# Performance work log

Measured on AMD Instinct MI355X. Metric: run time of the kernel, lower is better.

The kernel has to match this reference:

```python
import jax, jax.numpy as jnp
import numpy as np

B, S, D, H = 2, 2048, 1024, 16
HD = D // H
EPS = 1e-8
LN_EPS = 1e-5


def setup_inputs() -> dict:
    key = jax.random.key(0)
    ks = jax.random.split(key, 12)
    std = 0.02
    inp = {}
    inp["x"] = jax.random.normal(ks[0], (B, S, D), jnp.float32)
    # q/k/v/out projections (stored (in, out); y = x @ W + b)
    inp["Wq"] = jax.random.normal(ks[1], (D, D), jnp.float32) * std
    inp["bq"] = jnp.zeros((D,), jnp.float32)
    inp["Wk"] = jax.random.normal(ks[2], (D, D), jnp.float32) * std
    inp["bk"] = jnp.zeros((D,), jnp.float32)
    inp["Wv"] = jax.random.normal(ks[3], (D, D), jnp.float32) * std
    inp["bv"] = jnp.zeros((D,), jnp.float32)
    inp["Wo"] = jax.random.normal(ks[4], (D, D), jnp.float32) * std
    inp["bo"] = jnp.zeros((D,), jnp.float32)
    # 4 DeltaResidualBlocks stacked on axis 0: [q, k, v, out]
    inp["dWk"] = jax.random.normal(ks[5], (4, D, D), jnp.float32) * 0.01  # k_proj, no bias
    inp["dbw"] = jnp.zeros((4, D), jnp.float32)                           # beta_proj weight (init zeros)
    inp["dbb"] = jnp.full((4,), -4.0, jnp.float32)                        # beta_proj bias
    inp["dWv"] = jax.random.normal(ks[6], (4, D), jnp.float32) * 0.02     # v_proj weight (d_v=1)
    inp["dbv"] = jnp.zeros((4,), jnp.float32)                             # v_proj bias
    inp["ln_g"] = jnp.ones((D,), jnp.float32)
    inp["ln_b"] = jnp.zeros((D,), jnp.float32)
    return inp


def reference(x, Wq, bq, Wk, bk, Wv, bv, Wo, bo, dWk, dbw, dbb, dWv, dbv, ln_g, ln_b):
    def delta(h, v_in, i):
        # DeltaResidualBlock (d_v=1): h + beta * k * (v - k.h)
        k_raw = jnp.einsum('bsd,de->bse', h, dWk[i])
        k = k_raw / (jnp.linalg.norm(k_raw, axis=-1, keepdims=True) + EPS)
        beta = 2.0 * jax.nn.sigmoid(jnp.einsum('bsd,d->bs', h, dbw[i])[..., None] + dbb[i])  # (B,S,1)
        v = jnp.einsum('bsd,d->bs', v_in, dWv[i])[..., None] + dbv[i]                        # (B,S,1)
        k_dot_h = jnp.sum(k * h, axis=-1, keepdims=True)
        return h + beta * k * (v - k_dot_h)

    q = delta(x, x @ Wq + bq, 0)
    k = delta(x, x @ Wk + bk, 1)
    v = delta(x, x @ Wv + bv, 2)

    # (B,S,D) -> (B,H,S,HD)
    q = q.reshape(B, S, H, HD).transpose(0, 2, 1, 3)
    k = k.reshape(B, S, H, HD).transpose(0, 2, 1, 3)
    v = v.reshape(B, S, H, HD).transpose(0, 2, 1, 3)

    scale = HD ** -0.5
    scores = jnp.einsum('bhqd,bhkd->bhqk', q, k) * scale
    attn = jax.nn.softmax(scores, axis=-1)
    out = jnp.einsum('bhqk,bhkd->bhqd', attn, v)
    out = out.transpose(0, 2, 1, 3).reshape(B, S, D)
    out = out @ Wo + bo

    y = delta(x, out, 3)

    # LayerNorm
    mu = jnp.mean(y, axis=-1, keepdims=True)
    var = jnp.mean((y - mu) ** 2, axis=-1, keepdims=True)
    y = (y - mu) / jnp.sqrt(var + LN_EPS) * ln_g + ln_b
    return y
```

## Files before the change

### kernel.cpp

```cpp
#include <hip/hip_runtime.h>

#define BB 2
#define SS 2048
#define DD 1024
#define HH 16
#define HD 64
#define MM (BB*SS)
#define KC 4
#define KT_PER (SS/64/KC)
#define KSTEPS (DD/64)

typedef unsigned short u16;
typedef __attribute__((ext_vector_type(8))) short bf16x8;
typedef __attribute__((ext_vector_type(4))) float f32x4;

typedef __attribute__((address_space(1))) const unsigned int* gas_t;
typedef __attribute__((address_space(3))) unsigned int* las_t;

#ifndef __has_builtin
#define __has_builtin(x) 0
#endif
#if __has_builtin(__builtin_amdgcn_exp2f)
#define EXP2F(x) __builtin_amdgcn_exp2f(x)
#else
#define EXP2F(x) __expf((x)*0.6931471805599453f)
#endif
#define QSCALE 0.18033688011112042f

__device__ __forceinline__ void gl_lds16(const u16* g, u16* l){
  __builtin_amdgcn_global_load_lds((gas_t)g, (las_t)l, 16, 0, 0);
}

__device__ __forceinline__ u16 f2bf(float f){
  unsigned u = __float_as_uint(f);
  u += 0x7FFF + ((u >> 16) & 1);
  return (u16)(u >> 16);
}
__device__ __forceinline__ float bf2f(u16 h){
  return __uint_as_float(((unsigned)h) << 16);
}
__device__ __forceinline__ float dot4f(float4 a, float4 b){
  return a.x*b.x + a.y*b.y + a.z*b.z + a.w*b.w;
}

template <int CTRL>
__device__ __forceinline__ float dppadd(float x){
  int y = __builtin_amdgcn_update_dpp(0, __float_as_int(x), CTRL, 0xF, 0xF, true);
  return x + __int_as_float(y);
}
__device__ __forceinline__ float4 wsum64_f4(float4 v){
  #define DPP_ST(c) v.x=dppadd<c>(v.x); v.y=dppadd<c>(v.y); v.z=dppadd<c>(v.z); v.w=dppadd<c>(v.w);
  DPP_ST(0x111) DPP_ST(0x112) DPP_ST(0x114) DPP_ST(0x118) DPP_ST(0x142) DPP_ST(0x143)
  #undef DPP_ST
  return v;
}
__device__ __forceinline__ float2 wsum64_f2(float2 v){
  #define DPP_ST(c) v.x=dppadd<c>(v.x); v.y=dppadd<c>(v.y);
  DPP_ST(0x111) DPP_ST(0x112) DPP_ST(0x114) DPP_ST(0x118) DPP_ST(0x142) DPP_ST(0x143)
  #undef DPP_ST
  return v;
}

#define SB0() __builtin_amdgcn_sched_barrier(0)
#define SBAR() do { \
  __builtin_amdgcn_sched_barrier(0); \
  __builtin_amdgcn_s_barrier(); \
  __builtin_amdgcn_sched_barrier(0); \
} while (0)

#define NB_CONV 2048
#define NB_TRAN 1024
#define NB_PREC 4100
#define NB_PREP (NB_CONV+NB_TRAN+NB_PREC)
__global__ void prep_kernel(const float* __restrict__ x, u16* __restrict__ xb,
                            const float* __restrict__ dWk, u16* __restrict__ dWkT,
                            const float* __restrict__ Wq_, const float* __restrict__ bq_,
                            const float* __restrict__ Wk_, const float* __restrict__ bk_,
                            const float* __restrict__ Wv_, const float* __restrict__ bv_,
                            const float* __restrict__ Wo_, const float* __restrict__ bo_,
                            const float* __restrict__ dWv, const float* __restrict__ dbv,
                            float* __restrict__ wv, float* __restrict__ cv) {
  int blk = blockIdx.x, t = threadIdx.x;
  if (blk < NB_CONV) {
    size_t idx = ((size_t)blk*256 + t)*8;
    float4 a = *(const float4*)(x + idx);
    float4 b = *(const float4*)(x + idx + 4);
    union { u16 u[8]; uint4 v; } pk;
    pk.u[0]=f2bf(a.x); pk.u[1]=f2bf(a.y); pk.u[2]=f2bf(a.z); pk.u[3]=f2bf(a.w);
    pk.u[4]=f2bf(b.x); pk.u[5]=f2bf(b.y); pk.u[6]=f2bf(b.z); pk.u[7]=f2bf(b.w);
    *(uint4*)(xb + idx) = pk.v;
    return;
  }
  blk -= NB_CONV;
  if (blk < NB_TRAN) {
    int i = blk >> 8, rest = blk & 255;
    int k0 = (rest >> 4) << 6, n0 = (rest & 15) << 6;
    const float* src = dWk + (size_t)i*DD*DD;
    u16* dst = dWkT + (size_t)i*DD*DD;
    __shared__ u16 tr[64*68];
    const int krb = (t >> 4) << 2;
    const int nqb = (t & 15) << 2;
    float4 v0 = *(const float4*)(src + (size_t)(k0+krb+0)*DD + n0 + nqb);
    float4 v1 = *(const float4*)(src + (size_t)(k0+krb+1)*DD + n0 + nqb);
    float4 v2 = *(const float4*)(src + (size_t)(k0+krb+2)*DD + n0 + nqb);
    float4 v3 = *(const float4*)(src + (size_t)(k0+krb+3)*DD + n0 + nqb);
    *(uint2*)(&tr[(nqb+0)*68 + krb]) = make_uint2(
        (unsigned)f2bf(v0.x) | ((unsigned)f2bf(v1.x)<<16),
        (unsigned)f2bf(v2.x) | ((unsigned)f2bf(v3.x)<<16));
    *(uint2*)(&tr[(nqb+1)*68 + krb]) = make_uint2(
        (unsigned)f2bf(v0.y) | ((unsigned)f2bf(v1.y)<<16),
        (unsigned)f2bf(v2.y) | ((unsigned)f2bf(v3.y)<<16));
    *(uint2*)(&tr[(nqb+2)*68 + krb]) = make_uint2(
        (unsigned)f2bf(v0.z) | ((unsigned)f2bf(v1.z)<<16),
        (unsigned)f2bf(v2.z) | ((unsigned)f2bf(v3.z)<<16));
    *(uint2*)(&tr[(nqb+3)*68 + krb]) = make_uint2(
        (unsigned)f2bf(v0.w) | ((unsigned)f2bf(v1.w)<<16),
        (unsigned)f2bf(v2.w) | ((unsigned)f2bf(v3.w)<<16));
    __syncthreads();
    const int n = t >> 2, c = t & 3;
    uint2 r0 = *(uint2*)(&tr[n*68 + c*16 + 0]);
    uint2 r1 = *(uint2*)(&tr[n*68 + c*16 + 4]);
    uint2 r2 = *(uint2*)(&tr[n*68 + c*16 + 8]);
    uint2 r3 = *(uint2*)(&tr[n*68 + c*16 + 12]);
    u16* dp = dst + (size_t)(n0+n)*DD + k0 + c*16;
    *(uint4*)(dp + 0) = make_uint4(r0.x, r0.y, r1.x, r1.y);
    *(uint4*)(dp + 8) = make_uint4(r2.x, r2.y, r3.x, r3.y);
    return;
  }
  blk -= NB_TRAN;
  {
    int i = blk / 1025, row = blk % 1025;
    const float* W    = (i==0)?Wq_:(i==1)?Wk_:(i==2)?Wv_:Wo_;
    const float* bvec = (i==0)?bq_:(i==1)?bk_:(i==2)?bv_:bo_;
    const float* s = dWv + i*DD;
    __shared__ float red[256];
    float acc = 0.f;
    if (row < DD) {
      const float* r = W + (size_t)row * DD;
      for (int e = t; e < DD; e += 256) acc += r[e]*s[e];
    } else {
      for (int e = t; e < DD; e += 256) acc += bvec[e]*s[e];
    }
    red[t] = acc; __syncthreads();
    for (int off=128; off>0; off>>=1){ if(t<off) red[t]+=red[t+off]; __syncthreads(); }
    if (t==0) {
      if (row < DD) wv[i*DD + row] = red[0];
      else          cv[i] = red[0] + dbv[i];
    }
  }
}

__device__ __forceinline__ void stage_half(const u16* __restrict__ g, u16* l,
                                           int k0, int half, int isA,
                                           int wid, int lane) {
  const int lr = lane>>3, lc = lane&7;
  #pragma unroll
  for (int j=0; j<2; j++) {
    const int u = wid*2 + j;
    int grow;
    if (isA) grow = ((u & 8) ? 128 + ((u & 7)<<3) : (u<<3)) + (half<<6);
    else     grow = ((u>>2)<<6) + ((u&3)<<3) + (half<<5);
    gl_lds16(g + (size_t)(grow + lr)*DD + k0 + ((lc^lr)<<3), l + grow*64);
  }
}

__device__ __forceinline__ void lda4(const u16* base, int row0, int q15, int quad,
                                     int sw, bf16x8 (&f)[4][2]) {
  #pragma unroll
  for (int mf=0; mf<4; mf++)
    #pragma unroll
    for (int kk=0; kk<2; kk++)
      f[mf][kk] = *(const bf16x8*)(base + (row0 + mf*16 + q15)*64 + (((kk*4+quad)^sw)<<3));
}
__device__ __forceinline__ void ldb2(const u16* base, int row0, int q15, int quad,
                                     int sw, bf16x8 (&f)[2][2]) {
  #pragma unroll
  for (int nf=0; nf<2; nf++)
    #pragma unroll
    for (int kk=0; kk<2; kk++)
      f[nf][kk] = *(const bf16x8*)(base + (row0 + nf*16 + q15)*64 + (((kk*4+quad)^sw)<<3));
}
__device__ __forceinline__ void quad_mfma(const bf16x8 (&af)[4][2], const bf16x8 (&bfr)[2][2],
                                          f32x4 (&acc)[8][4], int mo, int no) {
  __builtin_amdgcn_s_setprio(1);
  #pragma unroll
  for (int kk=0; kk<2; kk++)
    #pragma unroll
    for (int mf=0; mf<4; mf++)
      #pragma unroll
      for (int nf=0; nf<2; nf++)
        acc[mo+mf][no+nf] = __builtin_amdgcn_mfma_f32_16x16x32_bf16(
            bfr[nf][kk], af[mf][kk], acc[mo+mf][no+nf], 0,0,0);
  __builtin_amdgcn_s_setprio(0);
}

__global__ __launch_bounds__(512, 2) void gemm_dwk_8ph(const u16* __restrict__ xb,
                          const u16* __restrict__ Bt, u16* __restrict__ kraw) {
  const int bid = blockIdx.x;
  const int xcd = bid & 7, rr = bid >> 3;
  const int i = xcd >> 1;
  const int mt = ((xcd & 1) << 3) | (rr & 7);
  const int ntile = rr >> 3;
  const int m0 = mt << 8, n0 = ntile << 8;
  const u16* Ab = xb + (size_t)m0*DD;
  const u16* Bb = Bt + (size_t)i*DD*DD + (size_t)n0*DD;
  u16* C = kraw + (size_t)i*MM*DD;

  const int t = threadIdx.x, wid = t>>6, lane = t&63;
  const int q15 = lane&15, quad = lane>>4, sw = q15&7;
  const int wm = wid>>2, wn = wid&3;
  const int arow = wm<<7, brow = wn<<6;

  __shared__ u16 As[2][256*64];
  __shared__ u16 Bs[2][256*64];

  f32x4 acc[8][4];
  #pragma unroll
  for (int a=0;a<8;a++)
    #pragma unroll
    for (int b2=0;b2<4;b2++) acc[a][b2] = (f32x4){0.f,0.f,0.f,0.f};

  stage_half(Ab, As[0], 0,  0, 1, wid, lane);
  stage_half(Bb, Bs[0], 0,  0, 0, wid, lane);
  stage_half(Bb, Bs[0], 0,  1, 0, wid, lane);
  stage_half(Ab, As[0], 0,  1, 1, wid, lane);
  stage_half(Ab, As[1], 64, 0, 1, wid, lane);
  stage_half(Bb, Bs[1], 64, 0, 0, wid, lane);
  stage_half(Bb, Bs[1], 64, 1, 0, wid, lane);
  SB0();
  asm volatile("s_waitcnt vmcnt(6)" ::: "memory");
  SBAR();

  for (int u=0; u<KSTEPS; ++u) {
    const int cur = u & 1;
    const u16* Ac = As[cur]; const u16* Bc = Bs[cur];
    const int k1 = (u+1 < KSTEPS ? u+1 : KSTEPS-1) << 6;
    const int k2 = (u+2 < KSTEPS ? u+2 : KSTEPS-1) << 6;
    bf16x8 a0[4][2], a1[4][2], b0[2][2], b1[2][2];

    lda4(Ac, arow,    q15, quad, sw, a0);
    ldb2(Bc, brow,    q15, quad, sw, b0);
    ldb2(Bc, brow+32, q15, quad, sw, b1);
    stage_half(Ab, As[cur^1], k1, 1, 1, wid, lane);
    SB0();
    quad_mfma(a0, b0, acc, 0, 0);
    quad_mfma(a0, b1, acc, 0, 2);
    SB0();
    lda4(Ac, arow+64, q15, quad, sw, a1);
    SB0();
    __builtin_amdgcn_s_barrier();
    SB0();
    stage_half(Ab, As[cur], k2, 0, 1, wid, lane);
    stage_half(Bb, Bs[cur], k2, 0, 0, wid, lane);
    stage_half(Bb, Bs[cur], k2, 1, 0, wid, lane);
    SB0();
    quad_mfma(a1, b1, acc, 4, 2);
    quad_mfma(a1, b0, acc, 4, 0);
    SB0();
    asm volatile("s_waitcnt vmcnt(6)" ::: "memory");
    __builtin_amdgcn_s_barrier();
    SB0();
  }

  #pragma unroll
  for (int mf=0; mf<8; mf++) {
    const int m = m0 + arow + mf*16 + q15;
    u16* Crow = C + (size_t)m*DD + n0 + brow;
    #pragma unroll
    for (int nf=0; nf<4; nf++) {
      unsigned u0 = (unsigned)f2bf(acc[mf][nf][0]) | ((unsigned)f2bf(acc[mf][nf][1]) << 16);
      unsigned u1 = (unsigned)f2bf(acc[mf][nf][2]) | ((unsigned)f2bf(acc[mf][nf][3]) << 16);
      *(uint2*)(Crow + nf*16 + quad*4) = make_uint2(u0, u1);
    }
  }
}

__global__ void delta_qkv_kernel(const float* __restrict__ x, const u16* __restrict__ kraw,
                                 const float* __restrict__ dbw, const float* __restrict__ dbb,
                                 const float* __restrict__ wv, const float* __restrict__ cv,
                                 u16* __restrict__ qk, float* __restrict__ Vw) {
  int m = blockIdx.x, t = threadIdx.x, w = t>>6, lane = t&63;
  const float* xr = x + (size_t)m*DD;
  float4 xv = *(const float4*)(xr + t*4);
  __shared__ float4 part[3][4];
  float4 kvs[3];
  #pragma unroll
  for (int i=0;i<3;i++) {
    ushort4 ku = *(const ushort4*)(kraw + (size_t)i*MM*DD + (size_t)m*DD + t*4);
    float4 kv = make_float4(bf2f(ku.x), bf2f(ku.y), bf2f(ku.z), bf2f(ku.w));
    kvs[i] = kv;
    float4 bwv = *(const float4*)(dbw + i*DD + t*4);
    float4 wvv = *(const float4*)(wv  + i*DD + t*4);
    float4 red = make_float4(dot4f(kv,kv), dot4f(kv,xv), dot4f(xv,bwv), dot4f(xv,wvv));
    red = wsum64_f4(red);
    if (lane==63) part[i][w] = red;
  }
  __syncthreads();
  float cc[3];
  #pragma unroll
  for (int i=0;i<3;i++) {
    float4 r0=part[i][0], r1=part[i][1], r2=part[i][2], r3=part[i][3];
    float s0=r0.x+r1.x+r2.x+r3.x, s1=r0.y+r1.y+r2.y+r3.y;
    float s2=r0.z+r1.z+r2.z+r3.z, s3=r0.w+r1.w+r2.w+r3.w;
    float nrmE = sqrtf(s0) + 1e-8f;
    float kdh  = s1 / nrmE;
    float beta = 2.f / (1.f + __expf(-(s2 + dbb[i])));
    float vs   = s3 + cv[i];
    cc[i] = beta * (vs - kdh) / nrmE;
  }
  {
    float c = cc[0]; float4 kv = kvs[0];
    ushort4 ou;
    ou.x = f2bf((xv.x + c*kv.x)*QSCALE); ou.y = f2bf((xv.y + c*kv.y)*QSCALE);
    ou.z = f2bf((xv.z + c*kv.z)*QSCALE); ou.w = f2bf((xv.w + c*kv.w)*QSCALE);
    *(ushort4*)(qk + (size_t)m*DD + t*4) = ou;
  }
  {
    float c = cc[1]; float4 kv = kvs[1];
    ushort4 ou;
    ou.x = f2bf(xv.x + c*kv.x); ou.y = f2bf(xv.y + c*kv.y);
    ou.z = f2bf(xv.z + c*kv.z); ou.w = f2bf(xv.w + c*kv.w);
    *(ushort4*)(qk + (size_t)MM*DD + (size_t)m*DD + t*4) = ou;
  }
  {
    float c = cc[2]; float4 kv = kvs[2];
    float4 vv = make_float4(xv.x + c*kv.x, xv.y + c*kv.y, xv.z + c*kv.z, xv.w + c*kv.w);
    float4 w3 = *(const float4*)(wv + 3*DD + t*4);
    float s = dot4f(vv, w3);
    #pragma unroll
    for (int off=1; off<16; off<<=1) s += __shfl_xor(s, off);
    if ((lane & 15) == 0) {
      int head = t >> 4;
      int b = m >> 11, srow = m & (SS-1);
      Vw[((size_t)(b*HH + head))*SS + srow] = s;
    }
  }
}

__global__ __launch_bounds__(256, 6) void flash_mfma(const u16* __restrict__ qb,
     const u16* __restrict__ kb, const float* __restrict__ Vw,
     float* __restrict__ l_arr, float* __restrict__ pv_arr) {
  const int qt = blockIdx.x, h = blockIdx.y;
  const int b = blockIdx.z >> 2, kc = blockIdx.z & 3;
  const int t = threadIdx.x, w = t>>6, lane = t&63, q15 = lane&15, quad = lane>>4;
  const int lr = lane>>3, lc = lane&7, gsw = lc ^ lr;
  const int sw = q15 & 7;
  __shared__ u16 Ks[3][64*64];
  __shared__ float Vws[KT_PER*64];
  const size_t hb = (size_t)h*HD;
  const u16* kbase = kb + (size_t)(b*SS + kc*KT_PER*64)*DD + hb;
  const float* vwb = Vw + (size_t)(b*HH + h)*SS + kc*KT_PER*64;

  bf16x8 qf[2];
  {
    const u16* qrow = qb + (size_t)(b*SS + qt*64 + w*16 + q15)*DD + hb;
    qf[0] = *(const bf16x8*)(qrow + quad*8);
    qf[1] = *(const bf16x8*)(qrow + 32 + quad*8);
  }
  if (t < KT_PER*64/4) {
    float4 v = *(const float4*)(vwb + t*4);
    *(float4*)(&Vws[t*4]) = v;
  }
  #pragma unroll
  for (int j=0; j<2; j++) {
    int r = (w*2+j)*8 + lr;
    gl_lds16(kbase + (size_t)r*DD + gsw*8, &Ks[0][((w*2+j)*8)*64]);
    gl_lds16(kbase + (size_t)(64 + r)*DD + gsw*8, &Ks[1][((w*2+j)*8)*64]);
  }
  float l_acc = 0.f, pv_acc = 0.f;
  __syncthreads();

  #pragma unroll
  for (int kt=0; kt<KT_PER; kt++) {
    if (kt+2 < KT_PER) {
      #pragma unroll
      for (int j=0; j<2; j++) {
        int r = (w*2+j)*8 + lr;
        gl_lds16(kbase + (size_t)((kt+2)*64 + r)*DD + gsw*8,
                 &Ks[(kt+2)%3][((w*2+j)*8)*64]);
      }
    }
    f32x4 Sacc[4];
    #pragma unroll
    for (int rt=0; rt<4; rt++) Sacc[rt] = (f32x4){0.f,0.f,0.f,0.f};
    #pragma unroll
    for (int kk=0; kk<2; kk++) {
      #pragma unroll
      for (int rt=0; rt<4; rt++) {
        bf16x8 kf = *(bf16x8*)(&Ks[kt%3][(rt*16+q15)*64 + ((kk*4+quad)^sw)*8]);
        Sacc[rt] = __builtin_amdgcn_mfma_f32_16x16x32_bf16(kf, qf[kk], Sacc[rt], 0,0,0);
      }
    }
    #pragma unroll
    for (int rt=0; rt<4; rt++) {
      float4 va = *(const float4*)(&Vws[kt*64 + rt*16 + quad*4]);
      float p0 = EXP2F(fminf(Sacc[rt][0], 30.f));
      float p1 = EXP2F(fminf(Sacc[rt][1], 30.f));
      float p2 = EXP2F(fminf(Sacc[rt][2], 30.f));
      float p3 = EXP2F(fminf(Sacc[rt][3], 30.f));
      l_acc  += (p0 + p1) + (p2 + p3);
      pv_acc += p0*va.x + p1*va.y + p2*va.z + p3*va.w;
    }
    if (kt < KT_PER-1) {
      __builtin_amdgcn_sched_barrier(0);
      if (kt+2 < KT_PER) asm volatile("s_waitcnt vmcnt(2)" ::: "memory");
      else               asm volatile("s_waitcnt vmcnt(0)" ::: "memory");
      __builtin_amdgcn_s_barrier();
      __builtin_amdgcn_sched_barrier(0);
    }
  }
  l_acc  += __shfl_xor(l_acc, 16);  l_acc  += __shfl_xor(l_acc, 32);
  pv_acc += __shfl_xor(pv_acc, 16); pv_acc += __shfl_xor(pv_acc, 32);
  if (quad == 0) {
    int tok = b*SS + qt*64 + w*16 + q15;
    size_t idx = ((size_t)kc*MM + tok)*HH + h;
    l_arr[idx]  = l_acc;
    pv_arr[idx] = pv_acc;
  }
}

__global__ void final_kernel(const float* __restrict__ x, const u16* __restrict__ kraw3,
                             const float* __restrict__ l_arr, const float* __restrict__ pv_arr,
                             const float* __restrict__ dbw, const float* __restrict__ dbb,
                             const float* __restrict__ cv,
                             const float* __restrict__ ln_g, const float* __restrict__ ln_b,
                             float* __restrict__ out) {
  int m = blockIdx.x, t = threadIdx.x, w = t>>6, lane = t&63;
  const float* xr = x     + (size_t)m*DD;
  const u16*   kr = kraw3 + (size_t)m*DD;
  float4 xv  = *(const float4*)(xr + t*4);
  ushort4 ku = *(const ushort4*)(kr + t*4);
  float4 kv  = make_float4(bf2f(ku.x), bf2f(ku.y), bf2f(ku.z), bf2f(ku.w));
  float4 bwv = *(const float4*)(dbw + 3*DD + t*4);
  __shared__ float4 part[4];
  __shared__ float2 part2[4];
  __shared__ float v3s;
  if (t < 16) {
    float lsum = 0.f, psum = 0.f;
    #pragma unroll
    for (int kc=0; kc<KC; kc++) {
      size_t idx = ((size_t)kc*MM + m)*HH + t;
      lsum += l_arr[idx];
      psum += pv_arr[idx];
    }
    float val = psum / lsum;
    #pragma unroll
    for (int off=1; off<16; off<<=1) val += __shfl_xor(val, off);
    if (t==0) v3s = val;
  }
  float4 red = make_float4(dot4f(kv,kv), dot4f(kv,xv), dot4f(xv,bwv), 0.f);
  red = wsum64_f4(red);
  if (lane==63) part[w] = red;
  __syncthreads();
  float4 r0=part[0], r1=part[1], r2=part[2], r3=part[3];
  float s0=r0.x+r1.x+r2.x+r3.x, s1=r0.y+r1.y+r2.y+r3.y, s2=r0.z+r1.z+r2.z+r3.z;
  float nrmE = sqrtf(s0) + 1e-8f;
  float kdh  = s1 / nrmE;
  float beta = 2.f / (1.f + __expf(-(s2 + dbb[3])));
  float v3   = v3s + cv[3];
  float c = beta * (v3 - kdh) / nrmE;
  float y0 = xv.x + c*kv.x, y1 = xv.y + c*kv.y, y2 = xv.z + c*kv.z, y3 = xv.w + c*kv.w;
  float2 rr = make_float2(y0+y1+y2+y3, y0*y0+y1*y1+y2*y2+y3*y3);
  rr = wsum64_f2(rr);
  if (lane==63) part2[w] = rr;
  __syncthreads();
  float ssum = part2[0].x+part2[1].x+part2[2].x+part2[3].x;
  float ssq  = part2[0].y+part2[1].y+part2[2].y+part2[3].y;
  float mu   = ssum * (1.f/DD);
  float var  = ssq * (1.f/DD) - mu*mu;
  float rstd = rsqrtf(var + 1e-5f);
  float4 g  = *(const float4*)(ln_g + t*4);
  float4 bb = *(const float4*)(ln_b + t*4);
  float4 ov;
  ov.x = (y0-mu)*rstd*g.x + bb.x;
  ov.y = (y1-mu)*rstd*g.y + bb.y;
  ov.z = (y2-mu)*rstd*g.z + bb.z;
  ov.w = (y3-mu)*rstd*g.w + bb.w;
  *(float4*)(out + (size_t)m*DD + t*4) = ov;
}

extern "C" void kernel_launch(void* const* d_in, const int* in_sizes, int n_in,
                              void* d_out, int out_size, void* d_ws, size_t ws_size,
                              hipStream_t stream) {
  const float* x    = (const float*)d_in[0];
  const float* Wq_  = (const float*)d_in[1];
  const float* bq_  = (const float*)d_in[2];
  const float* Wk_  = (const float*)d_in[3];
  const float* bk_  = (const float*)d_in[4];
  const float* Wv_  = (const float*)d_in[5];
  const float* bv_  = (const float*)d_in[6];
  const float* Wo_  = (const float*)d_in[7];
  const float* bo_  = (const float*)d_in[8];
  const float* dWk  = (const float*)d_in[9];
  const float* dbw  = (const float*)d_in[10];
  const float* dbb  = (const float*)d_in[11];
  const float* dWv  = (const float*)d_in[12];
  const float* dbv  = (const float*)d_in[13];
  const float* ln_g = (const float*)d_in[14];
  const float* ln_b = (const float*)d_in[15];
  float* out = (float*)d_out;
  char* WS = (char*)d_ws;

  float* wv     = (float*)WS;
  float* cv     = (float*)(WS + 16384);
  u16*   kraw   = (u16*)  (WS + 16640);
  u16*   qk     = (u16*)  (WS + 16640 + (size_t)4*MM*DD*2);
  u16*   dWkT   = (u16*)  (WS + 16640 + (size_t)6*MM*DD*2);
  u16*   xb     = (u16*)  (WS + 16640 + (size_t)6*MM*DD*2 + (size_t)4*DD*DD*2);
  char*  tail   = WS + 16640 + (size_t)6*MM*DD*2 + (size_t)8*DD*DD*2;
  float* Vw     = (float*)tail;
  float* l_arr  = (float*)(tail + (size_t)BB*HH*SS*4);
  float* pv_arr = (float*)(tail + (size_t)BB*HH*SS*4 + (size_t)KC*MM*HH*4);

  prep_kernel<<<NB_PREP, 256, 0, stream>>>(
      x, xb, dWk, dWkT, Wq_,bq_,Wk_,bk_,Wv_,bv_,Wo_,bo_, dWv, dbv, wv, cv);
  gemm_dwk_8ph<<<256, 512, 0, stream>>>(xb, dWkT, kraw);
  delta_qkv_kernel<<<MM, 256, 0, stream>>>(x, kraw, dbw, dbb, wv, cv, qk, Vw);
  flash_mfma<<<dim3(SS/64, HH, BB*KC), 256, 0, stream>>>(
      qk, qk + (size_t)MM*DD, Vw, l_arr, pv_arr);
  final_kernel<<<MM, 256, 0, stream>>>(x, kraw + 3*(size_t)MM*DD, l_arr, pv_arr,
                                       dbw, dbb, cv, ln_g, ln_b, out);
}
```

Before: 219.6 us.

## Split flash key tile across waves instead of query rows, reduce via LDS

Each wave now owns 16 keys of the 64-key tile and computes scores against all 64 query rows. It loads only two K fragments per step instead of eight, while holding four sets of Q fragments in registers. Per-row partial sums from the four waves are combined through shared memory before the global write. The aim is fewer LDS reads per MFMA, paid for with more registers, which is why the occupancy hint drops from 6 to 4 blocks, plus an extra barrier and reduction at the end.

```diff
diff --git a/kernel.cpp b/kernel.cpp
--- a/kernel.cpp
+++ b/kernel.cpp
@@ -337,7 +337,7 @@
   }
 }
 
-__global__ __launch_bounds__(256, 6) void flash_mfma(const u16* __restrict__ qb,
+__global__ __launch_bounds__(256, 4) void flash_mfma(const u16* __restrict__ qb,
      const u16* __restrict__ kb, const float* __restrict__ Vw,
      float* __restrict__ l_arr, float* __restrict__ pv_arr) {
   const int qt = blockIdx.x, h = blockIdx.y;
@@ -347,15 +347,17 @@
   const int sw = q15 & 7;
   __shared__ u16 Ks[3][64*64];
   __shared__ float Vws[KT_PER*64];
+  __shared__ float2 red2[4*64];
   const size_t hb = (size_t)h*HD;
   const u16* kbase = kb + (size_t)(b*SS + kc*KT_PER*64)*DD + hb;
   const float* vwb = Vw + (size_t)(b*HH + h)*SS + kc*KT_PER*64;
 
-  bf16x8 qf[2];
-  {
-    const u16* qrow = qb + (size_t)(b*SS + qt*64 + w*16 + q15)*DD + hb;
-    qf[0] = *(const bf16x8*)(qrow + quad*8);
-    qf[1] = *(const bf16x8*)(qrow + 32 + quad*8);
+  bf16x8 qf[4][2];
+  #pragma unroll
+  for (int qt2=0; qt2<4; qt2++) {
+    const u16* qrow = qb + (size_t)(b*SS + qt*64 + qt2*16 + q15)*DD + hb;
+    qf[qt2][0] = *(const bf16x8*)(qrow + quad*8);
+    qf[qt2][1] = *(const bf16x8*)(qrow + 32 + quad*8);
   }
   if (t < KT_PER*64/4) {
     float4 v = *(const float4*)(vwb + t*4);
@@ -367,7 +369,7 @@
     gl_lds16(kbase + (size_t)r*DD + gsw*8, &Ks[0][((w*2+j)*8)*64]);
     gl_lds16(kbase + (size_t)(64 + r)*DD + gsw*8, &Ks[1][((w*2+j)*8)*64]);
   }
-  float l_acc = 0.f, pv_acc = 0.f;
+  float l_acc[4] = {0.f,0.f,0.f,0.f}, pv_acc[4] = {0.f,0.f,0.f,0.f};
   __syncthreads();
 
   #pragma unroll
@@ -380,26 +382,25 @@
                  &Ks[(kt+2)%3][((w*2+j)*8)*64]);
       }
     }
+    bf16x8 kf0 = *(bf16x8*)(&Ks[kt%3][(w*16+q15)*64 + ((quad  )^sw)*8]);
+    bf16x8 kf1 = *(bf16x8*)(&Ks[kt%3][(w*16+q15)*64 + ((4+quad)^sw)*8]);
     f32x4 Sacc[4];
     #pragma unroll
-    for (int rt=0; rt<4; rt++) Sacc[rt] = (f32x4){0.f,0.f,0.f,0.f};
-    #pragma unroll
-    for (int kk=0; kk<2; kk++) {
-      #pragma unroll
-      for (int rt=0; rt<4; rt++) {
-        bf16x8 kf = *(bf16x8*)(&Ks[kt%3][(rt*16+q15)*64 + ((kk*4+quad)^sw)*8]);
-        Sacc[rt] = __builtin_amdgcn_mfma_f32_16x16x32_bf16(kf, qf[kk], Sacc[rt], 0,0,0);
-      }
-    }
-    #pragma unroll
-    for (int rt=0; rt<4; rt++) {
-      float4 va = *(const float4*)(&Vws[kt*64 + rt*16 + quad*4]);
-      float p0 = EXP2F(fminf(Sacc[rt][0], 30.f));
-      float p1 = EXP2F(fminf(Sacc[rt][1], 30.f));
-      float p2 = EXP2F(fminf(Sacc[rt][2], 30.f));
-      float p3 = EXP2F(fminf(Sacc[rt][3], 30.f));
-      l_acc  += (p0 + p1) + (p2 + p3);
-      pv_acc += p0*va.x + p1*va.y + p2*va.z + p3*va.w;
+    for (int qt2=0; qt2<4; qt2++) Sacc[qt2] = (f32x4){0.f,0.f,0.f,0.f};
+    #pragma unroll
+    for (int qt2=0; qt2<4; qt2++) {
+      Sacc[qt2] = __builtin_amdgcn_mfma_f32_16x16x32_bf16(kf0, qf[qt2][0], Sacc[qt2], 0,0,0);
+      Sacc[qt2] = __builtin_amdgcn_mfma_f32_16x16x32_bf16(kf1, qf[qt2][1], Sacc[qt2], 0,0,0);
+    }
+    float4 va = *(const float4*)(&Vws[kt*64 + w*16 + quad*4]);
+    #pragma unroll
+    for (int qt2=0; qt2<4; qt2++) {
+      float p0 = EXP2F(fminf(Sacc[qt2][0], 30.f));
+      float p1 = EXP2F(fminf(Sacc[qt2][1], 30.f));
+      float p2 = EXP2F(fminf(Sacc[qt2][2], 30.f));
+      float p3 = EXP2F(fminf(Sacc[qt2][3], 30.f));
+      l_acc[qt2]  += (p0 + p1) + (p2 + p3);
+      pv_acc[qt2] += p0*va.x + p1*va.y + p2*va.z + p3*va.w;
     }
     if (kt < KT_PER-1) {
       __builtin_amdgcn_sched_barrier(0);
@@ -409,13 +410,25 @@
       __builtin_amdgcn_sched_barrier(0);
     }
   }
-  l_acc  += __shfl_xor(l_acc, 16);  l_acc  += __shfl_xor(l_acc, 32);
-  pv_acc += __shfl_xor(pv_acc, 16); pv_acc += __shfl_xor(pv_acc, 32);
-  if (quad == 0) {
-    int tok = b*SS + qt*64 + w*16 + q15;
+  #pragma unroll
+  for (int qt2=0; qt2<4; qt2++) {
+    l_acc[qt2]  += __shfl_xor(l_acc[qt2], 16);  l_acc[qt2]  += __shfl_xor(l_acc[qt2], 32);
+    pv_acc[qt2] += __shfl_xor(pv_acc[qt2], 16); pv_acc[qt2] += __shfl_xor(pv_acc[qt2], 32);
+  }
+  if (lane < 16) {
+    #pragma unroll
+    for (int qt2=0; qt2<4; qt2++)
+      red2[w*64 + qt2*16 + lane] = make_float2(l_acc[qt2], pv_acc[qt2]);
+  }
+  __syncthreads();
+  if (t < 64) {
+    float2 p0 = red2[t], p1 = red2[64+t], p2 = red2[128+t], p3 = red2[192+t];
+    float ls = (p0.x+p1.x) + (p2.x+p3.x);
+    float ps = (p0.y+p1.y) + (p2.y+p3.y);
+    int tok = b*SS + qt*64 + t;
     size_t idx = ((size_t)kc*MM + tok)*HH + h;
-    l_arr[idx]  = l_acc;
-    pv_arr[idx] = pv_acc;
+    l_arr[idx]  = ls;
+    pv_arr[idx] = ps;
   }
 }
 
```

Result: slower. 263.3 us (+19.9%).
